# Optimization experiments

Hardware: AMD Instinct MI355X
Metric: run time of the kernel (lower is better)

## Reference

```python
import jax, jax.numpy as jnp
import numpy as np

B, C, H, W = 8, 3840, 32, 32
C8 = C // 8


def setup_inputs() -> dict:
    key = jax.random.key(0)
    ks = jax.random.split(key, 4)
    x = jax.random.normal(ks[0], (B, C, H, W), dtype=jnp.float32)
    Wq = jax.random.normal(ks[1], (C8, C), dtype=jnp.float32) * 0.02
    Wk = jax.random.normal(ks[2], (C8, C), dtype=jnp.float32) * 0.02
    Wv = jax.random.normal(ks[3], (C, C), dtype=jnp.float32) * 0.02
    bq = jnp.zeros((C8,), jnp.float32)
    bk = jnp.zeros((C8,), jnp.float32)
    bv = jnp.zeros((C,), jnp.float32)
    gamma = jnp.zeros((1,), jnp.float32)
    return {"x": x, "Wq": Wq, "bq": bq, "Wk": Wk, "bk": bk,
            "Wv": Wv, "bv": bv, "gamma": gamma}


def reference(x, Wq, bq, Wk, bk, Wv, bv, gamma):
    b, c, h, w = x.shape
    n = h * w
    xf = x.reshape(b, c, n)  # flatten spatial: (B, C, N)
    # 1x1 convs == per-pixel channel matmuls
    q = jnp.einsum('oc,bcn->bon', Wq, xf) + bq[None, :, None]   # (B, C/8, N)
    k = jnp.einsum('oc,bcn->bon', Wk, xf) + bk[None, :, None]   # (B, C/8, N)
    v = jnp.einsum('oc,bcn->bon', Wv, xf) + bv[None, :, None]   # (B, C,  N)
    # energy[b,i,j] = q[b,:,i] . k[b,:,j]  (no scaling, as in source)
    energy = jnp.einsum('bci,bcj->bij', q, k)                    # (B, N, N)
    attn = jax.nn.softmax(energy, axis=-1)
    # out[b,c,i] = sum_j v[b,c,j] * attn[b,i,j]
    out = jnp.einsum('bcj,bij->bci', v, attn).reshape(b, c, h, w)
    return out * gamma + x
```

## Files before the change

kernel.cpp:

```cpp
#include <hip/hip_runtime.h>
#include <stdint.h>


typedef __attribute__((ext_vector_type(4))) float f32x4;
typedef __attribute__((ext_vector_type(8))) short bf16x8;
typedef __attribute__((ext_vector_type(4))) short s16x4;

namespace {
constexpr int kB = 8, kC = 3840, kC8 = 480, kN = 1024;
constexpr int kM  = 4800;
constexpr int kMp = 4864;
constexpr int kNT = kB * kN;
}

__device__ __forceinline__ short f2bf(float f) {
    union { float f; uint32_t u; } v; v.f = f;
    return (short)((v.u + 0x7FFFu + ((v.u >> 16) & 1u)) >> 16);
}

__device__ __forceinline__ void gl16(const void* g, void* l) {
    __builtin_amdgcn_global_load_lds(
        (const __attribute__((address_space(1))) void*)g,
        (__attribute__((address_space(3))) void*)(uint32_t)(uintptr_t)l,
        16, 0, 0);
}

#define DSR(d, a, o) asm volatile("ds_read_b128 %0, %1 offset:" o \
    : "=v"(d) : "v"(a) : "memory")

__global__ __launch_bounds__(256)
void convert_wc(const float* __restrict__ Wq, const float* __restrict__ Wk,
                const float* __restrict__ Wv, short* __restrict__ Wc)
{
    const size_t g  = (size_t)blockIdx.x * 256 + threadIdx.x;
    const size_t e0 = g * 8;
    const int r = (int)(e0 / kC);
    const int c = (int)(e0 % kC);
    const float* src = nullptr;
    if (r < kC8)          src = Wq + (size_t)r * kC + c;
    else if (r < 2 * kC8) src = Wk + (size_t)(r - kC8) * kC + c;
    else if (r < kM)      src = Wv + (size_t)(r - 2 * kC8) * kC + c;
    bf16x8 o;
    if (src) {
        float4 a = *(const float4*)src;
        float4 b = *(const float4*)(src + 4);
        o[0]=f2bf(a.x); o[1]=f2bf(a.y); o[2]=f2bf(a.z); o[3]=f2bf(a.w);
        o[4]=f2bf(b.x); o[5]=f2bf(b.y); o[6]=f2bf(b.z); o[7]=f2bf(b.w);
    } else {
        o = (bf16x8)0;
    }
    *(bf16x8*)(Wc + e0) = o;
}

__global__ __launch_bounds__(256)
void convert_bias(const float* __restrict__ bq, const float* __restrict__ bk,
                  const float* __restrict__ bv, float* __restrict__ biasC)
{
    const int r = blockIdx.x * 256 + threadIdx.x;
    if (r >= kMp) return;
    biasC[r] = r < kC8 ? bq[r] : r < 2*kC8 ? bk[r - kC8] : r < kM ? bv[r - 2*kC8] : 0.f;
}

__global__ __launch_bounds__(256)
void transpose_x(const float* __restrict__ x, short* __restrict__ xbT)
{
    __shared__ float t[32][33];
    const int tid = threadIdx.x;
    const int b = blockIdx.z, c0 = blockIdx.y * 32, n0 = blockIdx.x * 32;
    const int r = tid >> 3, q4 = (tid & 7) * 4;
    float4 v = *(const float4*)(x + ((size_t)b * kC + c0 + r) * kN + n0 + q4);
    t[r][q4] = v.x; t[r][q4+1] = v.y; t[r][q4+2] = v.z; t[r][q4+3] = v.w;
    __syncthreads();
    s16x4 o;
    o[0] = f2bf(t[q4+0][r]); o[1] = f2bf(t[q4+1][r]);
    o[2] = f2bf(t[q4+2][r]); o[3] = f2bf(t[q4+3][r]);
    *(s16x4*)(xbT + (size_t)(b * kN + n0 + r) * kC + c0 + q4) = o;
}

__global__ __launch_bounds__(256)
void transpose_qk(const short* __restrict__ qkv, short* __restrict__ qT,
                  short* __restrict__ kT)
{
    __shared__ short t[32][36];
    const int tid = threadIdx.x;
    const int o0 = blockIdx.y * 32, bn0 = blockIdx.x * 32;
    const int r = tid >> 3, q4 = (tid & 7) * 4;
    s16x4 v = *(const s16x4*)(qkv + (size_t)(o0 + r) * kNT + bn0 + q4);
    t[r][q4] = v[0]; t[r][q4+1] = v[1]; t[r][q4+2] = v[2]; t[r][q4+3] = v[3];
    __syncthreads();
    s16x4 o;
    o[0] = t[q4+0][r]; o[1] = t[q4+1][r]; o[2] = t[q4+2][r]; o[3] = t[q4+3][r];
    const int oc = o0 + q4;
    short* dst = (o0 < kC8) ? (qT + (size_t)(bn0 + r) * kC8 + oc)
                            : (kT + (size_t)(bn0 + r) * kC8 + (oc - kC8));
    *(s16x4*)dst = o;
}

__global__ __launch_bounds__(256) void gemm_bt_e(
    const short* __restrict__ Abase, int lda,
    const short* __restrict__ Bbase, int ldb,
    int ksteps, long zsa, long zsb, long zso,
    float* __restrict__ eout)
{
    __shared__ __align__(16) short ldsA[128 * 32];
    __shared__ __align__(16) short ldsB[128 * 32];

    const int tid  = threadIdx.x;
    const int lane = tid & 63;
    const int w    = tid >> 6;
    const int m0 = blockIdx.y * 128;
    const int n0 = blockIdx.x * 128;
    const int z  = blockIdx.z;

    const char* Ab = (const char*)(Abase + (size_t)z * zsa);
    const char* Bb = (const char*)(Bbase + (size_t)z * zsb);
    const size_t ldab = (size_t)lda * 2, ldbb = (size_t)ldb * 2;

    const int srow  = w * 16 + (lane >> 2);
    const int scolb = (lane & 3) * 16;
    char* lA = (char*)ldsA;
    char* lB = (char*)ldsB;

    f32x4 acc[4][4];
#pragma unroll
    for (int i = 0; i < 4; ++i)
#pragma unroll
        for (int j = 0; j < 4; ++j) acc[i][j] = (f32x4)0.f;

    const int wm = (w >> 1) * 64, wn = (w & 1) * 64;
    const int fr = lane & 15;
    const int kb = (lane >> 4) * 16;

    for (int s = 0; s < ksteps; ++s) {
        const int k0b = s * 64;
        if (s) __syncthreads();
        gl16(Ab + (size_t)(m0 + srow)      * ldab + k0b + scolb, lA + w * 1024);
        gl16(Ab + (size_t)(m0 + 64 + srow) * ldab + k0b + scolb, lA + 4096 + w * 1024);
        gl16(Bb + (size_t)(n0 + srow)      * ldbb + k0b + scolb, lB + w * 1024);
        gl16(Bb + (size_t)(n0 + 64 + srow) * ldbb + k0b + scolb, lB + 4096 + w * 1024);
        __syncthreads();

        bf16x8 af[4], bfv[4];
#pragma unroll
        for (int f = 0; f < 4; ++f) {
            af[f]  = *(const bf16x8*)(lA + (wm + f * 16 + fr) * 64 + kb);
            bfv[f] = *(const bf16x8*)(lB + (wn + f * 16 + fr) * 64 + kb);
        }
#pragma unroll
        for (int fm = 0; fm < 4; ++fm)
#pragma unroll
            for (int fn = 0; fn < 4; ++fn)
                acc[fm][fn] = __builtin_amdgcn_mfma_f32_16x16x32_bf16(
                    af[fm], bfv[fn], acc[fm][fn], 0, 0, 0);
    }

    const int rbase = (lane >> 4) * 4;
    float* eb = eout + (size_t)z * zso;
#pragma unroll
    for (int fm = 0; fm < 4; ++fm)
#pragma unroll
        for (int fn = 0; fn < 4; ++fn)
#pragma unroll
            for (int r = 0; r < 4; ++r)
                eb[(size_t)(m0 + wm + fm*16 + rbase + r) * kN + (n0 + wn + fn*16 + fr)]
                    = acc[fm][fn][r];
}

template<int MODE>
__global__ __launch_bounds__(512) void gemm256(
    const short* __restrict__ Abase, int lda,
    const short* __restrict__ Bbase, int ldb,
    int ksteps, long zsa, long zsb, long zso,
    short* __restrict__ qkv, const float* __restrict__ biasC,
    const float* __restrict__ x, const float* __restrict__ gamma,
    float* __restrict__ out)
{
    __shared__ __align__(16) char lds[131072];

    const int tid  = threadIdx.x;
    const int lane = tid & 63;
    const int w    = tid >> 6;

    const int m0 = blockIdx.x * 256;
    const int n0 = blockIdx.y * 256;
    const int bz = blockIdx.z;

    const char* Ab = (const char*)(Abase + (size_t)bz * zsa);
    const char* Bb = (const char*)(Bbase + (size_t)bz * zsb);
    const size_t ldab = (size_t)lda * 2, ldbb = (size_t)ldb * 2;

    const int r8  = tid >> 3;
    const int scb = ((tid & 7) * 16) ^ ((r8 & 7) << 4);

#define STAGE(S, SLOTBASE)                                                     \
    do {                                                                       \
        const size_t kb_ = (size_t)(S) * 128;                                  \
        _Pragma("unroll")                                                      \
        for (int i_ = 0; i_ < 4; ++i_)                                         \
            gl16(Ab + (size_t)(m0 + r8 + 64 * i_) * ldab + kb_ + scb,          \
                 (SLOTBASE) + i_ * 8192 + w * 1024);                           \
        _Pragma("unroll")                                                      \
        for (int i_ = 0; i_ < 4; ++i_)                                         \
            gl16(Bb + (size_t)(n0 + r8 + 64 * i_) * ldbb + kb_ + scb,          \
                 (SLOTBASE) + 32768 + i_ * 8192 + w * 1024);                   \
    } while (0)

    const uint32_t lbase = (uint32_t)(uintptr_t)&lds[0];
    const int wr = w >> 2, wc = w & 3;
    const int fr = lane & 15, kq = lane >> 4;
    const uint32_t xorv = (uint32_t)((fr & 7) << 4);
    const uint32_t aoff0 = (uint32_t)((wr*128 + fr) * 128) + (((uint32_t)(kq*16)) ^ xorv);
    const uint32_t aoff1 = (uint32_t)((wr*128 + fr) * 128) + (((uint32_t)(64 + kq*16)) ^ xorv);
    const uint32_t boff0 = 32768u + (uint32_t)((wc*64 + fr) * 128) + (((uint32_t)(kq*16)) ^ xorv);
    const uint32_t boff1 = 32768u + (uint32_t)((wc*64 + fr) * 128) + (((uint32_t)(64 + kq*16)) ^ xorv);

    f32x4 acc[8][4];
#pragma unroll
    for (int i = 0; i < 8; ++i)
#pragma unroll
        for (int j = 0; j < 4; ++j) acc[i][j] = (f32x4)0.f;

    STAGE(0, lds);
    STAGE(1, lds + 65536);

    const int ns = ksteps;
    for (int s = 0; s < ns; ++s) {
        const uint32_t cur = (uint32_t)(s & 1);
        if (s + 1 < ns) asm volatile("s_waitcnt vmcnt(8)" ::: "memory");
        else            asm volatile("s_waitcnt vmcnt(0)" ::: "memory");
        __builtin_amdgcn_sched_barrier(0);
        __builtin_amdgcn_s_barrier();
        __builtin_amdgcn_sched_barrier(0);

        const uint32_t sb = lbase + cur * 65536u;
        const uint32_t aa0 = sb + aoff0, aa1 = sb + aoff1;
        const uint32_t bb0 = sb + boff0, bb1 = sb + boff1;

        bf16x8 b0v[4], b1v[4], a0[8], a1[8];
        DSR(b0v[0], bb0, "0");    DSR(b0v[1], bb0, "2048");
        DSR(b0v[2], bb0, "4096"); DSR(b0v[3], bb0, "6144");
        DSR(b1v[0], bb1, "0");    DSR(b1v[1], bb1, "2048");
        DSR(b1v[2], bb1, "4096"); DSR(b1v[3], bb1, "6144");
        DSR(a0[0], aa0, "0");    DSR(a0[1], aa0, "2048");
        DSR(a1[0], aa1, "0");    DSR(a1[1], aa1, "2048");
        DSR(a0[2], aa0, "4096"); DSR(a0[3], aa0, "6144");
        DSR(a1[2], aa1, "4096"); DSR(a1[3], aa1, "6144");

        asm volatile("s_waitcnt lgkmcnt(4)" ::: "memory");
        __builtin_amdgcn_sched_barrier(0);
        __builtin_amdgcn_s_setprio(1);
#pragma unroll
        for (int fm = 0; fm < 2; ++fm)
#pragma unroll
            for (int fn = 0; fn < 4; ++fn) {
                acc[fm][fn] = __builtin_amdgcn_mfma_f32_16x16x32_bf16(a0[fm], b0v[fn], acc[fm][fn], 0, 0, 0);
                acc[fm][fn] = __builtin_amdgcn_mfma_f32_16x16x32_bf16(a1[fm], b1v[fn], acc[fm][fn], 0, 0, 0);
            }
        __builtin_amdgcn_s_setprio(0);

        DSR(a0[4], aa0, "8192"); DSR(a0[5], aa0, "10240");
        DSR(a1[4], aa1, "8192"); DSR(a1[5], aa1, "10240");
        asm volatile("s_waitcnt lgkmcnt(4)" ::: "memory");
        __builtin_amdgcn_sched_barrier(0);
        __builtin_amdgcn_s_setprio(1);
#pragma unroll
        for (int fm = 2; fm < 4; ++fm)
#pragma unroll
            for (int fn = 0; fn < 4; ++fn) {
                acc[fm][fn] = __builtin_amdgcn_mfma_f32_16x16x32_bf16(a0[fm], b0v[fn], acc[fm][fn], 0, 0, 0);
                acc[fm][fn] = __builtin_amdgcn_mfma_f32_16x16x32_bf16(a1[fm], b1v[fn], acc[fm][fn], 0, 0, 0);
            }
        __builtin_amdgcn_s_setprio(0);

        DSR(a0[6], aa0, "12288"); DSR(a0[7], aa0, "14336");
        DSR(a1[6], aa1, "12288"); DSR(a1[7], aa1, "14336");
        asm volatile("s_waitcnt lgkmcnt(4)" ::: "memory");
        __builtin_amdgcn_sched_barrier(0);
        __builtin_amdgcn_s_setprio(1);
#pragma unroll
        for (int fm = 4; fm < 6; ++fm)
#pragma unroll
            for (int fn = 0; fn < 4; ++fn) {
                acc[fm][fn] = __builtin_amdgcn_mfma_f32_16x16x32_bf16(a0[fm], b0v[fn], acc[fm][fn], 0, 0, 0);
                acc[fm][fn] = __builtin_amdgcn_mfma_f32_16x16x32_bf16(a1[fm], b1v[fn], acc[fm][fn], 0, 0, 0);
            }
        __builtin_amdgcn_s_setprio(0);

        asm volatile("s_waitcnt lgkmcnt(0)" ::: "memory");
        __builtin_amdgcn_sched_barrier(0);
        __builtin_amdgcn_s_barrier();
        __builtin_amdgcn_sched_barrier(0);

        if (s + 2 < ns)
            STAGE(s + 2, lds + cur * 65536);
        __builtin_amdgcn_sched_barrier(0);

        __builtin_amdgcn_s_setprio(1);
#pragma unroll
        for (int fm = 6; fm < 8; ++fm)
#pragma unroll
            for (int fn = 0; fn < 4; ++fn) {
                acc[fm][fn] = __builtin_amdgcn_mfma_f32_16x16x32_bf16(a0[fm], b0v[fn], acc[fm][fn], 0, 0, 0);
                acc[fm][fn] = __builtin_amdgcn_mfma_f32_16x16x32_bf16(a1[fm], b1v[fn], acc[fm][fn], 0, 0, 0);
            }
        __builtin_amdgcn_s_setprio(0);
    }
#undef STAGE

    const int rbase = kq * 4;
    if (MODE == 0) {
#pragma unroll
        for (int fm = 0; fm < 8; ++fm) {
#pragma unroll
            for (int rr = 0; rr < 4; ++rr) {
                const int gm = m0 + wr * 128 + fm * 16 + rbase + rr;
                if (gm < kM) {
                    const float bias = biasC[gm];
#pragma unroll
                    for (int fn = 0; fn < 4; ++fn) {
                        const int gn = n0 + wc * 64 + fn * 16 + fr;
                        qkv[(size_t)gm * kNT + gn] = f2bf(acc[fm][fn][rr] + bias);
                    }
                }
            }
        }
    } else {
        const float g = gamma[0];
        const float* xb = x + (size_t)bz * zso;
        float* ob = out + (size_t)bz * zso;
#pragma unroll
        for (int fm = 0; fm < 8; ++fm)
#pragma unroll
            for (int fn = 0; fn < 4; ++fn)
#pragma unroll
                for (int rr = 0; rr < 4; ++rr) {
                    const size_t idx = (size_t)(m0 + wr*128 + fm*16 + rbase + rr) * kN
                                     + (n0 + wc*64 + fn*16 + fr);
                    ob[idx] = g * acc[fm][fn][rr] + xb[idx];
                }
    }
}

__global__ __launch_bounds__(256)
void softmax_bf(const float* __restrict__ e, short* __restrict__ attnb)
{
    const int i = blockIdx.x, b = blockIdx.y, tid = threadIdx.x;
    const float* row = e + ((size_t)b * kN + i) * kN;

    float4 vv = *(const float4*)(row + tid * 4);
    float m = fmaxf(fmaxf(vv.x, vv.y), fmaxf(vv.z, vv.w));

    __shared__ float red[8];
#pragma unroll
    for (int off = 32; off > 0; off >>= 1)
        m = fmaxf(m, __shfl_down(m, off));
    if ((tid & 63) == 0) red[tid >> 6] = m;
    __syncthreads();
    m = fmaxf(fmaxf(red[0], red[1]), fmaxf(red[2], red[3]));

    float e0 = expf(vv.x - m), e1 = expf(vv.y - m);
    float e2 = expf(vv.z - m), e3 = expf(vv.w - m);
    float s = e0 + e1 + e2 + e3;
#pragma unroll
    for (int off = 32; off > 0; off >>= 1)
        s += __shfl_down(s, off);
    if ((tid & 63) == 0) red[4 + (tid >> 6)] = s;
    __syncthreads();
    s = red[4] + red[5] + red[6] + red[7];

    const float inv = 1.0f / s;
    s16x4 o;
    o[0] = f2bf(e0 * inv); o[1] = f2bf(e1 * inv);
    o[2] = f2bf(e2 * inv); o[3] = f2bf(e3 * inv);
    *(s16x4*)(attnb + ((size_t)b * kN + i) * kN + tid * 4) = o;
}

extern "C" void kernel_launch(void* const* d_in, const int* in_sizes, int n_in,
                              void* d_out, int out_size, void* d_ws, size_t ws_size,
                              hipStream_t stream) {
    const float* x     = (const float*)d_in[0];
    const float* Wq    = (const float*)d_in[1];
    const float* bq    = (const float*)d_in[2];
    const float* Wk    = (const float*)d_in[3];
    const float* bk    = (const float*)d_in[4];
    const float* Wv    = (const float*)d_in[5];
    const float* bv    = (const float*)d_in[6];
    const float* gamma = (const float*)d_in[7];
    float* out = (float*)d_out;

    char* base = (char*)d_ws;
    short* xbT   = (short*)(base);
    short* attnb = (short*)(base);
    short* qT    = (short*)(base + 16777216);
    short* kT    = (short*)(base + 24641536);
    short* Wc    = (short*)(base + 62914560);
    float* attnf = (float*)(base + 62914560);
    float* biasC = (float*)(base + 100270080);
    short* qkv   = (short*)(base + 100289536);

    convert_wc  <<<9120, 256, 0, stream>>>(Wq, Wk, Wv, Wc);
    convert_bias<<<19, 256, 0, stream>>>(bq, bk, bv, biasC);
    transpose_x <<<dim3(32, 120, 8), 256, 0, stream>>>(x, xbT);

    gemm256<0><<<dim3(19, 32, 1), 512, 0, stream>>>(
        Wc, kC, xbT, kC, kC / 64, 0, 0, 0,
        qkv, biasC, nullptr, nullptr, nullptr);

    transpose_qk<<<dim3(256, 30, 1), 256, 0, stream>>>(qkv, qT, kT);

    gemm_bt_e<<<dim3(8, 8, 8), 256, 0, stream>>>(
        qT, kC8, kT, kC8, kC8 / 32,
        (long)kN * kC8, (long)kN * kC8, (long)kN * kN, attnf);

    softmax_bf<<<dim3(kN, kB), 256, 0, stream>>>(attnf, attnb);

    gemm256<2><<<dim3(15, 4, 8), 512, 0, stream>>>(
        qkv + (size_t)960 * kNT, kNT, attnb, kN, kN / 64,
        (long)kN, (long)kN * kN, (long)kC * kN,
        nullptr, nullptr, x, gamma, out);
}
```

Baseline: 514.6 us.

## Use 320-row tiles for QKV projection GEMM to remove M padding

The QKV projection GEMM now uses a dedicated kernel with 320x256 tiles, so M=4800 divides exactly into 15 row blocks instead of 19 padded 256-row blocks. This drops the 64 padded rows of wasted MFMA work and the padded weight/bias conversion, and reduces grid size from 608 to 480 blocks. The larger tile raises LDS use to 144KB and adds more accumulator registers (10x4 fragments), which may hurt occupancy or spill, and 480 blocks fit less evenly over the compute units.

Result: faster. 455.7 us, median of 2 (-11.5%).

```diff
diff --git a/kernel.cpp b/kernel.cpp
--- a/kernel.cpp
+++ b/kernel.cpp
@@ -9,7 +9,6 @@
 namespace {
 constexpr int kB = 8, kC = 3840, kC8 = 480, kN = 1024;
 constexpr int kM  = 4800;
-constexpr int kMp = 4864;
 constexpr int kNT = kB * kN;
 }
 
@@ -34,21 +33,18 @@
 {
     const size_t g  = (size_t)blockIdx.x * 256 + threadIdx.x;
     const size_t e0 = g * 8;
+    if (e0 >= (size_t)kM * kC) return;
     const int r = (int)(e0 / kC);
     const int c = (int)(e0 % kC);
-    const float* src = nullptr;
+    const float* src;
     if (r < kC8)          src = Wq + (size_t)r * kC + c;
     else if (r < 2 * kC8) src = Wk + (size_t)(r - kC8) * kC + c;
-    else if (r < kM)      src = Wv + (size_t)(r - 2 * kC8) * kC + c;
+    else                  src = Wv + (size_t)(r - 2 * kC8) * kC + c;
     bf16x8 o;
-    if (src) {
-        float4 a = *(const float4*)src;
-        float4 b = *(const float4*)(src + 4);
-        o[0]=f2bf(a.x); o[1]=f2bf(a.y); o[2]=f2bf(a.z); o[3]=f2bf(a.w);
-        o[4]=f2bf(b.x); o[5]=f2bf(b.y); o[6]=f2bf(b.z); o[7]=f2bf(b.w);
-    } else {
-        o = (bf16x8)0;
-    }
+    float4 a = *(const float4*)src;
+    float4 b = *(const float4*)(src + 4);
+    o[0]=f2bf(a.x); o[1]=f2bf(a.y); o[2]=f2bf(a.z); o[3]=f2bf(a.w);
+    o[4]=f2bf(b.x); o[5]=f2bf(b.y); o[6]=f2bf(b.z); o[7]=f2bf(b.w);
     *(bf16x8*)(Wc + e0) = o;
 }
 
@@ -57,8 +53,8 @@
                   const float* __restrict__ bv, float* __restrict__ biasC)
 {
     const int r = blockIdx.x * 256 + threadIdx.x;
-    if (r >= kMp) return;
-    biasC[r] = r < kC8 ? bq[r] : r < 2*kC8 ? bk[r - kC8] : r < kM ? bv[r - 2*kC8] : 0.f;
+    if (r >= kM) return;
+    biasC[r] = r < kC8 ? bq[r] : r < 2*kC8 ? bk[r - kC8] : bv[r - 2*kC8];
 }
 
 __global__ __launch_bounds__(256)
@@ -166,12 +162,170 @@
                     = acc[fm][fn][r];
 }
 
-template<int MODE>
-__global__ __launch_bounds__(512) void gemm256(
+__global__ __launch_bounds__(512) void gemm320(
+    const short* __restrict__ Wc, const short* __restrict__ xbT,
+    short* __restrict__ qkv, const float* __restrict__ biasC)
+{
+    __shared__ __align__(16) char lds[147456];
+
+    const int tid  = threadIdx.x;
+    const int lane = tid & 63;
+    const int w    = tid >> 6;
+    const int m0 = blockIdx.x * 320;
+    const int n0 = blockIdx.y * 256;
+
+    const char* Ab = (const char*)Wc;
+    const char* Bb = (const char*)xbT;
+    const size_t ldab = (size_t)kC * 2, ldbb = (size_t)kC * 2;
+
+    const int r8  = tid >> 3;
+    const int scb = ((tid & 7) * 16) ^ ((r8 & 7) << 4);
+
+#define STAGE320(S, SLOTBASE)                                                  \
+    do {                                                                       \
+        const size_t kb_ = (size_t)(S) * 128;                                  \
+        _Pragma("unroll")                                                      \
+        for (int p_ = 0; p_ < 5; ++p_)                                         \
+            gl16(Ab + (size_t)(m0 + p_ * 64 + r8) * ldab + kb_ + scb,          \
+                 (SLOTBASE) + p_ * 8192 + w * 1024);                           \
+        _Pragma("unroll")                                                      \
+        for (int p_ = 0; p_ < 4; ++p_)                                         \
+            gl16(Bb + (size_t)(n0 + p_ * 64 + r8) * ldbb + kb_ + scb,          \
+                 (SLOTBASE) + 40960 + p_ * 8192 + w * 1024);                   \
+    } while (0)
+
+    const uint32_t lbase = (uint32_t)(uintptr_t)&lds[0];
+    const int wr = w >> 2, wc = w & 3;
+    const int fr = lane & 15, kq = lane >> 4;
+    const uint32_t xorv = (uint32_t)((fr & 7) << 4);
+    const uint32_t kcol0 = ((uint32_t)(kq * 16)) ^ xorv;
+    const uint32_t kcol1 = ((uint32_t)(64 + kq * 16)) ^ xorv;
+    const uint32_t aoff0 = (uint32_t)((wr * 160 + fr) * 128) + kcol0;
+    const uint32_t aoff1 = (uint32_t)((wr * 160 + fr) * 128) + kcol1;
+    const uint32_t boff0 = 40960u + (uint32_t)((wc * 64 + fr) * 128) + kcol0;
+    const uint32_t boff1 = 40960u + (uint32_t)((wc * 64 + fr) * 128) + kcol1;
+
+    f32x4 acc[10][4];
+#pragma unroll
+    for (int i = 0; i < 10; ++i)
+#pragma unroll
+        for (int j = 0; j < 4; ++j) acc[i][j] = (f32x4)0.f;
+
+    STAGE320(0, lds);
+    STAGE320(1, lds + 73728);
+
+    const int ns = kC / 64;
+    for (int s = 0; s < ns; ++s) {
+        if (s + 1 < ns) asm volatile("s_waitcnt vmcnt(9)" ::: "memory");
+        else            asm volatile("s_waitcnt vmcnt(0)" ::: "memory");
+        __builtin_amdgcn_s_barrier();
+
+        const uint32_t sb = lbase + (uint32_t)(s & 1) * 73728u;
+        const uint32_t aa0 = sb + aoff0, aa1 = sb + aoff1;
+        const uint32_t bb0 = sb + boff0, bb1 = sb + boff1;
+
+        bf16x8 b0v[4], b1v[4], a0[10], a1[10];
+        DSR(b0v[0], bb0, "0");    DSR(b0v[1], bb0, "2048");
+        DSR(b0v[2], bb0, "4096"); DSR(b0v[3], bb0, "6144");
+        DSR(b1v[0], bb1, "0");    DSR(b1v[1], bb1, "2048");
+        DSR(b1v[2], bb1, "4096"); DSR(b1v[3], bb1, "6144");
+        DSR(a0[0], aa0, "0");     DSR(a1[0], aa1, "0");
+        DSR(a0[1], aa0, "2048");  DSR(a1[1], aa1, "2048");
+
+        DSR(a0[2], aa0, "4096");  DSR(a1[2], aa1, "4096");
+        DSR(a0[3], aa0, "6144");  DSR(a1[3], aa1, "6144");
+        asm volatile("s_waitcnt lgkmcnt(4)" ::: "memory");
+        __builtin_amdgcn_sched_barrier(0);
+        __builtin_amdgcn_s_setprio(1);
+#pragma unroll
+        for (int fm = 0; fm < 2; ++fm)
+#pragma unroll
+            for (int fn = 0; fn < 4; ++fn) {
+                acc[fm][fn] = __builtin_amdgcn_mfma_f32_16x16x32_bf16(a0[fm], b0v[fn], acc[fm][fn], 0, 0, 0);
+                acc[fm][fn] = __builtin_amdgcn_mfma_f32_16x16x32_bf16(a1[fm], b1v[fn], acc[fm][fn], 0, 0, 0);
+            }
+        __builtin_amdgcn_s_setprio(0);
+
+        DSR(a0[4], aa0, "8192");  DSR(a1[4], aa1, "8192");
+        DSR(a0[5], aa0, "10240"); DSR(a1[5], aa1, "10240");
+        asm volatile("s_waitcnt lgkmcnt(4)" ::: "memory");
+        __builtin_amdgcn_sched_barrier(0);
+        __builtin_amdgcn_s_setprio(1);
+#pragma unroll
+        for (int fm = 2; fm < 4; ++fm)
+#pragma unroll
+            for (int fn = 0; fn < 4; ++fn) {
+                acc[fm][fn] = __builtin_amdgcn_mfma_f32_16x16x32_bf16(a0[fm], b0v[fn], acc[fm][fn], 0, 0, 0);
+                acc[fm][fn] = __builtin_amdgcn_mfma_f32_16x16x32_bf16(a1[fm], b1v[fn], acc[fm][fn], 0, 0, 0);
+            }
+        __builtin_amdgcn_s_setprio(0);
+
+        DSR(a0[6], aa0, "12288"); DSR(a1[6], aa1, "12288");
+        DSR(a0[7], aa0, "14336"); DSR(a1[7], aa1, "14336");
+        asm volatile("s_waitcnt lgkmcnt(4)" ::: "memory");
+        __builtin_amdgcn_sched_barrier(0);
+        __builtin_amdgcn_s_setprio(1);
+#pragma unroll
+        for (int fm = 4; fm < 6; ++fm)
+#pragma unroll
+            for (int fn = 0; fn < 4; ++fn) {
+                acc[fm][fn] = __builtin_amdgcn_mfma_f32_16x16x32_bf16(a0[fm], b0v[fn], acc[fm][fn], 0, 0, 0);
+                acc[fm][fn] = __builtin_amdgcn_mfma_f32_16x16x32_bf16(a1[fm], b1v[fn], acc[fm][fn], 0, 0, 0);
+            }
+        __builtin_amdgcn_s_setprio(0);
+
+        DSR(a0[8], aa0, "16384"); DSR(a1[8], aa1, "16384");
+        DSR(a0[9], aa0, "18432"); DSR(a1[9], aa1, "18432");
+        asm volatile("s_waitcnt lgkmcnt(4)" ::: "memory");
+        __builtin_amdgcn_sched_barrier(0);
+        __builtin_amdgcn_s_setprio(1);
+#pragma unroll
+        for (int fm = 6; fm < 8; ++fm)
+#pragma unroll
+            for (int fn = 0; fn < 4; ++fn) {
+                acc[fm][fn] = __builtin_amdgcn_mfma_f32_16x16x32_bf16(a0[fm], b0v[fn], acc[fm][fn], 0, 0, 0);
+                acc[fm][fn] = __builtin_amdgcn_mfma_f32_16x16x32_bf16(a1[fm], b1v[fn], acc[fm][fn], 0, 0, 0);
+            }
+        __builtin_amdgcn_s_setprio(0);
+
+        asm volatile("s_waitcnt lgkmcnt(0)" ::: "memory");
+        __builtin_amdgcn_sched_barrier(0);
+        __builtin_amdgcn_s_barrier();
+        if (s + 2 < ns)
+            STAGE320(s + 2, lds + (size_t)(s & 1) * 73728);
+        __builtin_amdgcn_sched_barrier(0);
+        __builtin_amdgcn_s_setprio(1);
+#pragma unroll
+        for (int fm = 8; fm < 10; ++fm)
+#pragma unroll
+            for (int fn = 0; fn < 4; ++fn) {
+                acc[fm][fn] = __builtin_amdgcn_mfma_f32_16x16x32_bf16(a0[fm], b0v[fn], acc[fm][fn], 0, 0, 0);
+                acc[fm][fn] = __builtin_amdgcn_mfma_f32_16x16x32_bf16(a1[fm], b1v[fn], acc[fm][fn], 0, 0, 0);
+            }
+        __builtin_amdgcn_s_setprio(0);
+    }
+#undef STAGE320
+
+    const int rbase = kq * 4;
+#pragma unroll
+    for (int fm = 0; fm < 10; ++fm) {
+#pragma unroll
+        for (int rr = 0; rr < 4; ++rr) {
+            const int gm = m0 + wr * 160 + fm * 16 + rbase + rr;
+            const float bias = biasC[gm];
+#pragma unroll
+            for (int fn = 0; fn < 4; ++fn) {
+                const int gn = n0 + wc * 64 + fn * 16 + fr;
+                qkv[(size_t)gm * kNT + gn] = f2bf(acc[fm][fn][rr] + bias);
+            }
+        }
+    }
+}
+
+__global__ __launch_bounds__(512) void gemm256pv(
     const short* __restrict__ Abase, int lda,
     const short* __restrict__ Bbase, int ldb,
     int ksteps, long zsa, long zsb, long zso,
-    short* __restrict__ qkv, const float* __restrict__ biasC,
     const float* __restrict__ x, const float* __restrict__ gamma,
     float* __restrict__ out)
 {
@@ -308,37 +462,19 @@
 #undef STAGE
 
     const int rbase = kq * 4;
-    if (MODE == 0) {
-#pragma unroll
-        for (int fm = 0; fm < 8; ++fm) {
+    const float g = gamma[0];
+    const float* xb = x + (size_t)bz * zso;
+    float* ob = out + (size_t)bz * zso;
+#pragma unroll
+    for (int fm = 0; fm < 8; ++fm)
+#pragma unroll
+        for (int fn = 0; fn < 4; ++fn)
 #pragma unroll
             for (int rr = 0; rr < 4; ++rr) {
-                const int gm = m0 + wr * 128 + fm * 16 + rbase + rr;
-                if (gm < kM) {
-                    const float bias = biasC[gm];
-#pragma unroll
-                    for (int fn = 0; fn < 4; ++fn) {
-                        const int gn = n0 + wc * 64 + fn * 16 + fr;
-                        qkv[(size_t)gm * kNT + gn] = f2bf(acc[fm][fn][rr] + bias);
-                    }
-                }
-            }
-        }
-    } else {
-        const float g = gamma[0];
-        const float* xb = x + (size_t)bz * zso;
-        float* ob = out + (size_t)bz * zso;
-#pragma unroll
-        for (int fm = 0; fm < 8; ++fm)
-#pragma unroll
-            for (int fn = 0; fn < 4; ++fn)
-#pragma unroll
-                for (int rr = 0; rr < 4; ++rr) {
-                    const size_t idx = (size_t)(m0 + wr*128 + fm*16 + rbase + rr) * kN
-                                     + (n0 + wc*64 + fn*16 + fr);
-                    ob[idx] = g * acc[fm][fn][rr] + xb[idx];
-                }
-    }
+                const size_t idx = (size_t)(m0 + wr*128 + fm*16 + rbase + rr) * kN
+                                 + (n0 + wc*64 + fn*16 + fr);
+                ob[idx] = g * acc[fm][fn][rr] + xb[idx];
+            }
 }
 
 __global__ __launch_bounds__(256)
@@ -398,13 +534,11 @@
     float* biasC = (float*)(base + 100270080);
     short* qkv   = (short*)(base + 100289536);
 
-    convert_wc  <<<9120, 256, 0, stream>>>(Wq, Wk, Wv, Wc);
+    convert_wc  <<<9000, 256, 0, stream>>>(Wq, Wk, Wv, Wc);
     convert_bias<<<19, 256, 0, stream>>>(bq, bk, bv, biasC);
     transpose_x <<<dim3(32, 120, 8), 256, 0, stream>>>(x, xbT);
 
-    gemm256<0><<<dim3(19, 32, 1), 512, 0, stream>>>(
-        Wc, kC, xbT, kC, kC / 64, 0, 0, 0,
-        qkv, biasC, nullptr, nullptr, nullptr);
+    gemm320<<<dim3(15, 32), 512, 0, stream>>>(Wc, xbT, qkv, biasC);
 
     transpose_qk<<<dim3(256, 30, 1), 256, 0, stream>>>(qkv, qT, kT);
 
@@ -414,8 +548,8 @@
 
     softmax_bf<<<dim3(kN, kB), 256, 0, stream>>>(attnf, attnb);
 
-    gemm256<2><<<dim3(15, 4, 8), 512, 0, stream>>>(
+    gemm256pv<<<dim3(15, 4, 8), 512, 0, stream>>>(
         qkv + (size_t)960 * kNT, kNT, attnb, kN, kN / 64,
         (long)kN, (long)kN * kN, (long)kC * kN,
-        nullptr, nullptr, x, gamma, out);
-}
+        x, gamma, out);
+}
```
